# Kernel optimization log

Measured on AMD Instinct MI355X. Metric: run time of the kernel, lower is better.

Reference implementation:

```python
import jax, jax.numpy as jnp
import numpy as np
from jax import lax

NSAMPLE = 16
NEG_SLOPE = 0.1


def leaky(x):
    return jnp.where(x >= 0, x, NEG_SLOPE * x)


def setup_inputs() -> dict:
    key = jax.random.key(0)
    ks = jax.random.split(key, 8)
    B, N1, N2, D = 4, 4096, 4096, 64
    C_in, C_mid, C_out = D + D + 3, 128, 128  # 131 -> 128 -> 128
    xyz1 = jax.random.normal(ks[0], (B, 3, N1), jnp.float32)
    xyz2 = jax.random.normal(ks[1], (B, 3, N2), jnp.float32)
    points1 = jax.random.normal(ks[2], (B, D, N1), jnp.float32)
    points2 = jax.random.normal(ks[3], (B, D, N2), jnp.float32)
    W1 = jax.random.normal(ks[4], (C_mid, C_in), jnp.float32) * 0.05
    b1 = jnp.zeros((C_mid,), jnp.float32)
    W2 = jax.random.normal(ks[5], (C_out, C_mid), jnp.float32) * 0.05
    b2 = jnp.zeros((C_out,), jnp.float32)
    return {"xyz1": xyz1, "xyz2": xyz2, "points1": points1, "points2": points2,
            "W1": W1, "b1": b1, "W2": W2, "b2": b2}


def reference(xyz1, xyz2, points1, points2, W1, b1, W2, b2):
    B, _, N1 = xyz1.shape
    x1 = jnp.transpose(xyz1, (0, 2, 1))      # [B,N1,3]
    x2 = jnp.transpose(xyz2, (0, 2, 1))      # [B,N2,3]
    p1 = jnp.transpose(points1, (0, 2, 1))   # [B,N1,D1]
    p2 = jnp.transpose(points2, (0, 2, 1))   # [B,N2,D2]

    # knn_point: k smallest squared distances from each x1 point into x2
    d2 = (jnp.sum(x1 * x1, -1)[:, :, None]
          + jnp.sum(x2 * x2, -1)[:, None, :]
          - 2.0 * jnp.einsum('bnc,bmc->bnm', x1, x2))  # [B,N1,N2]
    _, knn_idx = lax.top_k(-d2, NSAMPLE)     # [B,N1,K]

    bidx = jnp.arange(B)[:, None, None]
    neighbor_xyz = x2[bidx, knn_idx]         # [B,N1,K,3]
    direction_xyz = neighbor_xyz - x1[:, :, None, :]
    gp2 = p2[bidx, knn_idx]                  # [B,N1,K,D2]
    gp1 = jnp.broadcast_to(p1[:, :, None, :], (B, N1, NSAMPLE, p1.shape[-1]))
    feat = jnp.concatenate([gp1, gp2, direction_xyz], axis=-1)  # [B,N1,K,131]

    h = leaky(jnp.einsum('oc,bnkc->bnko', W1, feat) + b1)
    h = leaky(jnp.einsum('oc,bnkc->bnko', W2, h) + b2)           # [B,N1,K,C_out]

    dist = jnp.maximum(jnp.linalg.norm(direction_xyz, axis=3), 1e-10)  # [B,N1,K]
    inv = 1.0 / dist
    weights = inv / jnp.sum(inv, axis=2, keepdims=True)          # [B,N1,K]

    cost = jnp.einsum('bnk,bnko->bon', weights, h)               # [B,C_out,N1]
    return cost
```

## Files before the change

kernel.cpp:

```cpp
#include <hip/hip_runtime.h>

typedef unsigned short u16;
typedef unsigned int u32;
typedef unsigned long long u64;
typedef __bf16 bf16x8 __attribute__((ext_vector_type(8)));
typedef float f32x4 __attribute__((ext_vector_type(4)));

#define MFMA16(a, b, c) __builtin_amdgcn_mfma_f32_16x16x32_bf16(a, b, c, 0, 0, 0)

static __device__ __forceinline__ u16 f2bf(float f) {
  union { float f; u32 u; } v; v.f = f;
  u32 u = v.u;
  u32 r = (u + 0x7FFFu + ((u >> 16) & 1u)) >> 16;
  return (u16)r;
}

static __device__ __forceinline__ bf16x8 ld16(const u16* p) {
  return __builtin_bit_cast(bf16x8, *(const uint4*)p);
}

static __device__ __forceinline__ u64 u64min(u64 a, u64 b) { return a < b ? a : b; }

static __device__ __forceinline__ u64 bitonic64(u64 v, int lane) {
#pragma unroll
  for (int k = 2; k <= 64; k <<= 1) {
#pragma unroll
    for (int j = k >> 1; j > 0; j >>= 1) {
      u64 o = __shfl_xor(v, j, 64);
      bool up = ((lane & k) == 0);
      bool lower = ((lane & j) == 0);
      u64 mn = v < o ? v : o;
      u64 mx = v < o ? o : v;
      v = (lower == up) ? mn : mx;
    }
  }
  return v;
}

__global__ __launch_bounds__(256) void transpose_cast(const float* __restrict__ src,
                                                      u16* __restrict__ dst) {
  __shared__ __align__(4) u16 tile[64 * 66];
  const int t = threadIdx.x;
  const int b = blockIdx.x >> 6;
  const int n0 = (blockIdx.x & 63) << 6;
  const float* sp = src + ((size_t)b << 18);
#pragma unroll
  for (int i = 0; i < 16; i++) {
    int d = (i << 2) + (t >> 6);
    int n = t & 63;
    tile[n * 66 + d] = f2bf(sp[((size_t)d << 12) + n0 + n]);
  }
  __syncthreads();
  u16* dp = dst + ((size_t)(b * 4096 + n0) << 6);
#pragma unroll
  for (int i = 0; i < 8; i++) {
    int n = (i << 3) + (t >> 5);
    int dp2 = t & 31;
    *(u32*)(dp + n * 64 + (dp2 << 1)) = *(const u32*)(tile + n * 66 + (dp2 << 1));
  }
}

__global__ __launch_bounds__(256) void prep_w(const float* __restrict__ W1,
                                              const float* __restrict__ W2,
                                              u16* __restrict__ W1b,
                                              u16* __restrict__ W2b) {
  int t = blockIdx.x * 256 + threadIdx.x;
  if (t < 128 * 160) {
    int r = t / 160, c = t - r * 160;
    W1b[t] = (c < 131) ? f2bf(W1[r * 131 + c]) : (u16)0;
  } else {
    int u = t - 128 * 160;
    W2b[u] = f2bf(W2[u]);
  }
}

__global__ __launch_bounds__(256) void s2_prep(const float* __restrict__ xyz2,
                                               float* __restrict__ s2) {
  int i = blockIdx.x * 256 + threadIdx.x;
  int b = i >> 12, m = i & 4095;
  const float* X2 = xyz2 + b * 12288;
  float bx = X2[m], by = X2[4096 + m], bz = X2[8192 + m];
  s2[i] = __fadd_rn(__fadd_rn(__fmul_rn(bx, bx), __fmul_rn(by, by)),
                    __fmul_rn(bz, bz));
}

__global__ __launch_bounds__(256, 2) void knn_kernel(const float* __restrict__ xyz1,
                                                     const float* __restrict__ xyz2,
                                                     const float* __restrict__ s2p,
                                                     int* __restrict__ knn) {
  __shared__ float bxL[4096], byL[4096], bzL[4096];
  __shared__ u64 surv[4][64];
  __shared__ u32 cnt[4];
  const int t = threadIdx.x;
  const int lane = t & 63;
  const int w = t >> 6;
  const int b = blockIdx.x >> 7;
  const int rbase = (blockIdx.x & 127) << 5;
  const float* X1 = xyz1 + b * 12288;
  const float* X2 = xyz2 + b * 12288;
  const float* S2 = s2p + b * 4096;

#pragma unroll
  for (int i = 0; i < 4; i++) {
    int e = (i * 256 + t) * 4;
    *(f32x4*)&bxL[e] = *(const f32x4*)&X2[e];
    *(f32x4*)&byL[e] = *(const f32x4*)&X2[4096 + e];
    *(f32x4*)&bzL[e] = *(const f32x4*)&X2[8192 + e];
  }
  __syncthreads();

#pragma unroll 1
  for (int r = 0; r < 8; r++) {
    const int n = rbase + (w << 3) + r;
    const int row = b * 4096 + n;
    const float x = X1[n];
    const float y = X1[4096 + n];
    const float z = X1[8192 + n];
    const float s1 = __fadd_rn(__fadd_rn(__fmul_rn(x, x), __fmul_rn(y, y)),
                               __fmul_rn(z, z));

    u32 keys[64];
    u64 head = ~0ull;
#pragma unroll
    for (int j = 0; j < 64; j++) {
      const int m = (j << 6) + lane;
      float bxv = bxL[m], byv = byL[m], bzv = bzL[m];
      float s2v = S2[m];
      float dt = __builtin_fmaf(z, bzv, __builtin_fmaf(y, byv, __fmul_rn(x, bxv)));
      float d2 = __fsub_rn(__fadd_rn(s1, s2v), __fmul_rn(2.0f, dt));
      u32 bb = __float_as_uint(d2);
      u32 sgn = (u32)((int)bb >> 31);
      u32 key = bb ^ (sgn | 0x80000000u);
      keys[j] = key;
      u64 k64 = ((u64)key << 32) | (u32)m;
      head = head < k64 ? head : k64;
    }

    u64 hs = bitonic64(head, lane);
    u64 tau = __shfl(hs, 15, 64);

    if (lane == 0) cnt[w] = 0;
#pragma unroll
    for (int j = 0; j < 64; j++) {
      u64 k64 = ((u64)keys[j] << 32) | (u32)((j << 6) + lane);
      if (k64 <= tau) {
        u32 slot = atomicAdd(&cnt[w], 1u);
        if (slot < 64) surv[w][slot] = k64;
      }
    }
    u32 S = cnt[w];

    if (S <= 64) {
      u64 v = (lane < (int)S) ? surv[w][lane] : ~0ull;
      v = bitonic64(v, lane);
      if (lane < 16) knn[row * 16 + lane] = (int)(v & 0xFFFFFFFFull);
    } else {
      u64 prev = 0;
      for (int rr = 0; rr < 16; rr++) {
        u64 lm = ~0ull;
#pragma unroll
        for (int j = 0; j < 64; j++) {
          u64 k64 = ((u64)keys[j] << 32) | (u32)((j << 6) + lane);
          if (k64 > prev && k64 < lm) lm = k64;
        }
        u64 gm = lm;
#pragma unroll
        for (int off = 32; off; off >>= 1) gm = u64min(gm, __shfl_xor(gm, off, 64));
        if (lane == 0) knn[row * 16 + rr] = (int)(gm & 0xFFFFFFFFull);
        prev = gm;
      }
    }
  }
}

__global__ __launch_bounds__(256, 3) void mlp_kernel(
    const float* __restrict__ xyz1, const float* __restrict__ xyz2,
    const u16* __restrict__ p1t, const u16* __restrict__ p2t,
    const int* __restrict__ knn,
    const u16* __restrict__ W1b, const float* __restrict__ b1,
    const u16* __restrict__ W2b, const float* __restrict__ b2,
    float* __restrict__ out) {
  __shared__ __align__(16) u16 F[128 * 168];
  __shared__ __align__(16) float winv[128];
  __shared__ __align__(16) float wnorm[128];
  __shared__ __align__(16) float outbuf[128 * 12];
  const int t = threadIdx.x;
  const int g = blockIdx.x;
  const int b = g >> 9;
  const int rbase = (g & 511) << 3;

  {
    const int m = t >> 1, half = t & 1;
    const int n1 = rbase + (m >> 4);
    const uint4* s1p = (const uint4*)(p1t + ((size_t)(b * 4096 + n1) << 6)) + half * 4;
    uint4* d1p = (uint4*)(F + m * 168) + half * 4;
    d1p[0] = s1p[0]; d1p[1] = s1p[1]; d1p[2] = s1p[2]; d1p[3] = s1p[3];
    const int idx = knn[(((size_t)(b * 4096 + n1)) << 4) + (m & 15)];
    const uint4* s2p = (const uint4*)(p2t + ((size_t)(b * 4096 + idx) << 6)) + half * 4;
    uint4* d2p = (uint4*)(F + m * 168 + 64) + half * 4;
    d2p[0] = s2p[0]; d2p[1] = s2p[1]; d2p[2] = s2p[2]; d2p[3] = s2p[3];
  }
  if (t < 128) {
    const int m = t;
    const int n1 = rbase + (m >> 4);
    const int idx = knn[(((size_t)(b * 4096 + n1)) << 4) + (m & 15)];
    const float* X1 = xyz1 + b * 12288;
    const float* X2 = xyz2 + b * 12288;
    float dx = X2[idx] - X1[n1];
    float dy = X2[4096 + idx] - X1[4096 + n1];
    float dz = X2[8192 + idx] - X1[8192 + n1];
    u32 u0 = (u32)f2bf(dx) | ((u32)f2bf(dy) << 16);
    u32 u1 = (u32)f2bf(dz);
    uint4 pk = make_uint4(u0, u1, 0u, 0u);
    *(uint4*)(F + m * 168 + 128) = pk;
    float d = sqrtf(dx * dx + dy * dy + dz * dz);
    winv[m] = 1.0f / fmaxf(d, 1e-10f);
  } else {
    const int m = t - 128;
    uint4 zz = make_uint4(0u, 0u, 0u, 0u);
    uint4* zp = (uint4*)(F + m * 168 + 136);
    zp[0] = zz; zp[1] = zz; zp[2] = zz; zp[3] = zz;
  }
  __syncthreads();

  if (t < 128) {
    const int r = t >> 4;
    float s = 0.f;
#pragma unroll
    for (int k = 0; k < 16; k++) s += winv[(r << 4) + k];
    wnorm[t] = winv[t] / s;
  }

  const int lane = t & 63;
  const int wid = t >> 6;
  const int l15 = lane & 15;
  const int quad = lane >> 4;
  const int koff = quad << 3;
  const int nbase = wid << 5;

  f32x4 acc[8][2];
  const f32x4 z4 = {0.f, 0.f, 0.f, 0.f};
#pragma unroll
  for (int i = 0; i < 8; i++)
#pragma unroll
    for (int j = 0; j < 2; j++) acc[i][j] = z4;

#pragma unroll
  for (int s = 0; s < 5; s++) {
    bf16x8 bf0 = ld16(W1b + (nbase + l15) * 160 + s * 32 + koff);
    bf16x8 bf1 = ld16(W1b + (nbase + 16 + l15) * 160 + s * 32 + koff);
#pragma unroll
    for (int mt = 0; mt < 8; mt++) {
      bf16x8 a = ld16(F + (mt * 16 + l15) * 168 + s * 32 + koff);
      acc[mt][0] = MFMA16(a, bf0, acc[mt][0]);
      acc[mt][1] = MFMA16(a, bf1, acc[mt][1]);
    }
  }
  __syncthreads();

  {
    const float bv0 = b1[nbase + l15];
    const float bv1 = b1[nbase + 16 + l15];
#pragma unroll
    for (int mt = 0; mt < 8; mt++) {
      u16* hrow = F + (mt * 16 + quad * 4) * 168;
#pragma unroll
      for (int r = 0; r < 4; r++) {
        float zv0 = acc[mt][0][r] + bv0;
        zv0 = (zv0 >= 0.f) ? zv0 : 0.1f * zv0;
        hrow[r * 168 + nbase + l15] = f2bf(zv0);
        float zv1 = acc[mt][1][r] + bv1;
        zv1 = (zv1 >= 0.f) ? zv1 : 0.1f * zv1;
        hrow[r * 168 + nbase + 16 + l15] = f2bf(zv1);
      }
    }
  }
  __syncthreads();

  f32x4 acc2[8][2];
#pragma unroll
  for (int i = 0; i < 8; i++)
#pragma unroll
    for (int j = 0; j < 2; j++) acc2[i][j] = z4;

#pragma unroll
  for (int s = 0; s < 4; s++) {
    bf16x8 bf0 = ld16(W2b + (nbase + l15) * 128 + s * 32 + koff);
    bf16x8 bf1 = ld16(W2b + (nbase + 16 + l15) * 128 + s * 32 + koff);
#pragma unroll
    for (int mt = 0; mt < 8; mt++) {
      bf16x8 a = ld16(F + (mt * 16 + l15) * 168 + s * 32 + koff);
      acc2[mt][0] = MFMA16(a, bf0, acc2[mt][0]);
      acc2[mt][1] = MFMA16(a, bf1, acc2[mt][1]);
    }
  }

  {
    const float bv0 = b2[nbase + l15];
    const float bv1 = b2[nbase + 16 + l15];
#pragma unroll
    for (int mt = 0; mt < 8; mt++) {
      const f32x4 w4 = *(const f32x4*)&wnorm[(mt << 4) + (quad << 2)];
      float p0 = 0.f, p1 = 0.f;
#pragma unroll
      for (int r = 0; r < 4; r++) {
        float zv0 = acc2[mt][0][r] + bv0;
        zv0 = (zv0 >= 0.f) ? zv0 : 0.1f * zv0;
        p0 += zv0 * w4[r];
        float zv1 = acc2[mt][1][r] + bv1;
        zv1 = (zv1 >= 0.f) ? zv1 : 0.1f * zv1;
        p1 += zv1 * w4[r];
      }
      p0 += __shfl_xor(p0, 16); p0 += __shfl_xor(p0, 32);
      p1 += __shfl_xor(p1, 16); p1 += __shfl_xor(p1, 32);
      if (quad == 0) {
        outbuf[(nbase + l15) * 12 + mt] = p0;
        outbuf[(nbase + 16 + l15) * 12 + mt] = p1;
      }
    }
  }
  __syncthreads();
  {
    const int ch = t >> 1, half = t & 1;
    f32x4 v = *(const f32x4*)&outbuf[ch * 12 + (half << 2)];
    float* op = out + (((size_t)(b * 128 + ch)) << 12) + rbase + (half << 2);
    *(f32x4*)op = v;
  }
}

extern "C" void kernel_launch(void* const* d_in, const int* in_sizes, int n_in,
                              void* d_out, int out_size, void* d_ws, size_t ws_size,
                              hipStream_t stream) {
  const float* xyz1 = (const float*)d_in[0];
  const float* xyz2 = (const float*)d_in[1];
  const float* points1 = (const float*)d_in[2];
  const float* points2 = (const float*)d_in[3];
  const float* W1 = (const float*)d_in[4];
  const float* b1 = (const float*)d_in[5];
  const float* W2 = (const float*)d_in[6];
  const float* b2 = (const float*)d_in[7];
  float* out = (float*)d_out;

  char* ws = (char*)d_ws;
  int* knn = (int*)ws;
  u16* p1t = (u16*)(ws + 1048576);
  u16* p2t = (u16*)(ws + 3145728);
  u16* W1b = (u16*)(ws + 5242880);
  u16* W2b = (u16*)(ws + 5283840);
  float* s2 = (float*)(ws + 5316608);

  hipLaunchKernelGGL(transpose_cast, dim3(256), dim3(256), 0, stream, points1, p1t);
  hipLaunchKernelGGL(transpose_cast, dim3(256), dim3(256), 0, stream, points2, p2t);
  hipLaunchKernelGGL(prep_w, dim3(144), dim3(256), 0, stream, W1, W2, W1b, W2b);
  hipLaunchKernelGGL(s2_prep, dim3(64), dim3(256), 0, stream, xyz2, s2);
  hipLaunchKernelGGL(knn_kernel, dim3(512), dim3(256), 0, stream, xyz1, xyz2, s2, knn);
  hipLaunchKernelGGL(mlp_kernel, dim3(2048), dim3(256), 0, stream,
                     xyz1, xyz2, p1t, p2t, knn, W1b, b1, W2b, b2, out);
}
```

Baseline: 174.1 us.

## Process two query rows per pass in knn with packed float4 candidates

Fuses the squared-norm precompute into the knn kernel and stores candidates in shared memory as packed (x,y,z,s2) float4. Each wave now computes distances for two query points per pass, so every shared-memory load serves two rows. Threshold selection uses a float bitonic sort instead of a 64-bit one. This doubles the per-thread key arrays, which raises register pressure and may reduce occupancy.

```diff
diff --git a/kernel.cpp b/kernel.cpp
--- a/kernel.cpp
+++ b/kernel.cpp
@@ -35,6 +35,34 @@
     }
   }
   return v;
+}
+
+static __device__ __forceinline__ float bitonic64f(float v, int lane) {
+#pragma unroll
+  for (int k = 2; k <= 64; k <<= 1) {
+#pragma unroll
+    for (int j = k >> 1; j > 0; j >>= 1) {
+      float o = __shfl_xor(v, j, 64);
+      bool up = ((lane & k) == 0);
+      bool lower = ((lane & j) == 0);
+      float mn = fminf(v, o);
+      float mx = fmaxf(v, o);
+      v = (lower == up) ? mn : mx;
+    }
+  }
+  return v;
+}
+
+static __device__ __forceinline__ u32 fkey(float f) {
+  u32 bb = __float_as_uint(f);
+  u32 sgn = (u32)((int)bb >> 31);
+  return bb ^ (sgn | 0x80000000u);
+}
+
+static __device__ __forceinline__ float d2of(float x, float y, float z, float s1,
+                                             f32x4 c) {
+  float dt = __builtin_fmaf(z, c[2], __builtin_fmaf(y, c[1], __fmul_rn(x, c[0])));
+  return __fsub_rn(__fadd_rn(s1, c[3]), __fmul_rn(2.0f, dt));
 }
 
 __global__ __launch_bounds__(256) void transpose_cast(const float* __restrict__ src,
@@ -74,21 +102,10 @@
   }
 }
 
-__global__ __launch_bounds__(256) void s2_prep(const float* __restrict__ xyz2,
-                                               float* __restrict__ s2) {
-  int i = blockIdx.x * 256 + threadIdx.x;
-  int b = i >> 12, m = i & 4095;
-  const float* X2 = xyz2 + b * 12288;
-  float bx = X2[m], by = X2[4096 + m], bz = X2[8192 + m];
-  s2[i] = __fadd_rn(__fadd_rn(__fmul_rn(bx, bx), __fmul_rn(by, by)),
-                    __fmul_rn(bz, bz));
-}
-
 __global__ __launch_bounds__(256, 2) void knn_kernel(const float* __restrict__ xyz1,
                                                      const float* __restrict__ xyz2,
-                                                     const float* __restrict__ s2p,
                                                      int* __restrict__ knn) {
-  __shared__ float bxL[4096], byL[4096], bzL[4096];
+  __shared__ __align__(16) float candL[4096 * 4];
   __shared__ u64 surv[4][64];
   __shared__ u32 cnt[4];
   const int t = threadIdx.x;
@@ -98,76 +115,107 @@
   const int rbase = (blockIdx.x & 127) << 5;
   const float* X1 = xyz1 + b * 12288;
   const float* X2 = xyz2 + b * 12288;
-  const float* S2 = s2p + b * 4096;
-
-#pragma unroll
-  for (int i = 0; i < 4; i++) {
-    int e = (i * 256 + t) * 4;
-    *(f32x4*)&bxL[e] = *(const f32x4*)&X2[e];
-    *(f32x4*)&byL[e] = *(const f32x4*)&X2[4096 + e];
-    *(f32x4*)&bzL[e] = *(const f32x4*)&X2[8192 + e];
+
+#pragma unroll
+  for (int j2 = 0; j2 < 16; j2++) {
+    int m = j2 * 256 + t;
+    float x = X2[m], y = X2[4096 + m], z = X2[8192 + m];
+    float s2 = __fadd_rn(__fadd_rn(__fmul_rn(x, x), __fmul_rn(y, y)),
+                         __fmul_rn(z, z));
+    f32x4 pk = {x, y, z, s2};
+    *(f32x4*)&candL[m * 4] = pk;
   }
   __syncthreads();
 
 #pragma unroll 1
-  for (int r = 0; r < 8; r++) {
-    const int n = rbase + (w << 3) + r;
-    const int row = b * 4096 + n;
-    const float x = X1[n];
-    const float y = X1[4096 + n];
-    const float z = X1[8192 + n];
-    const float s1 = __fadd_rn(__fadd_rn(__fmul_rn(x, x), __fmul_rn(y, y)),
-                               __fmul_rn(z, z));
-
-    u32 keys[64];
-    u64 head = ~0ull;
+  for (int p = 0; p < 4; p++) {
+    const int nA = rbase + (w << 3) + p * 2;
+    const int nB = nA + 1;
+    const float xA = X1[nA], yA = X1[4096 + nA], zA = X1[8192 + nA];
+    const float xB = X1[nB], yB = X1[4096 + nB], zB = X1[8192 + nB];
+    const float s1A = __fadd_rn(__fadd_rn(__fmul_rn(xA, xA), __fmul_rn(yA, yA)),
+                                __fmul_rn(zA, zA));
+    const float s1B = __fadd_rn(__fadd_rn(__fmul_rn(xB, xB), __fmul_rn(yB, yB)),
+                                __fmul_rn(zB, zB));
+
+    float kA[64], kB[64];
+    float fmA = 3e38f, fmB = 3e38f;
 #pragma unroll
     for (int j = 0; j < 64; j++) {
       const int m = (j << 6) + lane;
-      float bxv = bxL[m], byv = byL[m], bzv = bzL[m];
-      float s2v = S2[m];
-      float dt = __builtin_fmaf(z, bzv, __builtin_fmaf(y, byv, __fmul_rn(x, bxv)));
-      float d2 = __fsub_rn(__fadd_rn(s1, s2v), __fmul_rn(2.0f, dt));
-      u32 bb = __float_as_uint(d2);
-      u32 sgn = (u32)((int)bb >> 31);
-      u32 key = bb ^ (sgn | 0x80000000u);
-      keys[j] = key;
-      u64 k64 = ((u64)key << 32) | (u32)m;
-      head = head < k64 ? head : k64;
-    }
-
-    u64 hs = bitonic64(head, lane);
-    u64 tau = __shfl(hs, 15, 64);
-
-    if (lane == 0) cnt[w] = 0;
-#pragma unroll
-    for (int j = 0; j < 64; j++) {
-      u64 k64 = ((u64)keys[j] << 32) | (u32)((j << 6) + lane);
-      if (k64 <= tau) {
-        u32 slot = atomicAdd(&cnt[w], 1u);
-        if (slot < 64) surv[w][slot] = k64;
-      }
-    }
-    u32 S = cnt[w];
-
-    if (S <= 64) {
-      u64 v = (lane < (int)S) ? surv[w][lane] : ~0ull;
-      v = bitonic64(v, lane);
-      if (lane < 16) knn[row * 16 + lane] = (int)(v & 0xFFFFFFFFull);
-    } else {
-      u64 prev = 0;
-      for (int rr = 0; rr < 16; rr++) {
-        u64 lm = ~0ull;
-#pragma unroll
-        for (int j = 0; j < 64; j++) {
-          u64 k64 = ((u64)keys[j] << 32) | (u32)((j << 6) + lane);
-          if (k64 > prev && k64 < lm) lm = k64;
+      f32x4 c = *(const f32x4*)&candL[m * 4];
+      float dA = d2of(xA, yA, zA, s1A, c);
+      float dB = d2of(xB, yB, zB, s1B, c);
+      kA[j] = dA; fmA = fminf(fmA, dA);
+      kB[j] = dB; fmB = fminf(fmB, dB);
+    }
+
+    {
+      float tauf = __shfl(bitonic64f(fmA, lane), 15, 64);
+      if (lane == 0) cnt[w] = 0;
+#pragma unroll
+      for (int j = 0; j < 64; j++) {
+        if (kA[j] <= tauf) {
+          u64 k64 = ((u64)fkey(kA[j]) << 32) | (u32)((j << 6) + lane);
+          u32 slot = atomicAdd(&cnt[w], 1u);
+          if (slot < 64) surv[w][slot] = k64;
         }
-        u64 gm = lm;
-#pragma unroll
-        for (int off = 32; off; off >>= 1) gm = u64min(gm, __shfl_xor(gm, off, 64));
-        if (lane == 0) knn[row * 16 + rr] = (int)(gm & 0xFFFFFFFFull);
-        prev = gm;
+      }
+      u32 S = cnt[w];
+      const int row = b * 4096 + nA;
+      if (S <= 64) {
+        u64 v = (lane < (int)S) ? surv[w][lane] : ~0ull;
+        v = bitonic64(v, lane);
+        if (lane < 16) knn[row * 16 + lane] = (int)(v & 0xFFFFFFFFull);
+      } else {
+        u64 prev = 0;
+        for (int rr = 0; rr < 16; rr++) {
+          u64 lm = ~0ull;
+#pragma unroll
+          for (int j = 0; j < 64; j++) {
+            u64 k64 = ((u64)fkey(kA[j]) << 32) | (u32)((j << 6) + lane);
+            if (k64 > prev && k64 < lm) lm = k64;
+          }
+          u64 gm = lm;
+#pragma unroll
+          for (int off = 32; off; off >>= 1) gm = u64min(gm, __shfl_xor(gm, off, 64));
+          if (lane == 0) knn[row * 16 + rr] = (int)(gm & 0xFFFFFFFFull);
+          prev = gm;
+        }
+      }
+    }
+    {
+      float tauf = __shfl(bitonic64f(fmB, lane), 15, 64);
+      if (lane == 0) cnt[w] = 0;
+#pragma unroll
+      for (int j = 0; j < 64; j++) {
+        if (kB[j] <= tauf) {
+          u64 k64 = ((u64)fkey(kB[j]) << 32) | (u32)((j << 6) + lane);
+          u32 slot = atomicAdd(&cnt[w], 1u);
+          if (slot < 64) surv[w][slot] = k64;
+        }
+      }
+      u32 S = cnt[w];
+      const int row = b * 4096 + nB;
+      if (S <= 64) {
+        u64 v = (lane < (int)S) ? surv[w][lane] : ~0ull;
+        v = bitonic64(v, lane);
+        if (lane < 16) knn[row * 16 + lane] = (int)(v & 0xFFFFFFFFull);
+      } else {
+        u64 prev = 0;
+        for (int rr = 0; rr < 16; rr++) {
+          u64 lm = ~0ull;
+#pragma unroll
+          for (int j = 0; j < 64; j++) {
+            u64 k64 = ((u64)fkey(kB[j]) << 32) | (u32)((j << 6) + lane);
+            if (k64 > prev && k64 < lm) lm = k64;
+          }
+          u64 gm = lm;
+#pragma unroll
+          for (int off = 32; off; off >>= 1) gm = u64min(gm, __shfl_xor(gm, off, 64));
+          if (lane == 0) knn[row * 16 + rr] = (int)(gm & 0xFFFFFFFFull);
+          prev = gm;
+        }
       }
     }
   }
@@ -347,13 +395,11 @@
   u16* p2t = (u16*)(ws + 3145728);
   u16* W1b = (u16*)(ws + 5242880);
   u16* W2b = (u16*)(ws + 5283840);
-  float* s2 = (float*)(ws + 5316608);
 
   hipLaunchKernelGGL(transpose_cast, dim3(256), dim3(256), 0, stream, points1, p1t);
   hipLaunchKernelGGL(transpose_cast, dim3(256), dim3(256), 0, stream, points2, p2t);
   hipLaunchKernelGGL(prep_w, dim3(144), dim3(256), 0, stream, W1, W2, W1b, W2b);
-  hipLaunchKernelGGL(s2_prep, dim3(64), dim3(256), 0, stream, xyz2, s2);
-  hipLaunchKernelGGL(knn_kernel, dim3(512), dim3(256), 0, stream, xyz1, xyz2, s2, knn);
+  hipLaunchKernelGGL(knn_kernel, dim3(512), dim3(256), 0, stream, xyz1, xyz2, knn);
   hipLaunchKernelGGL(mlp_kernel, dim3(2048), dim3(256), 0, stream,
                      xyz1, xyz2, p1t, p2t, knn, W1b, b1, W2b, b2, out);
 }
```

After: 274.1 us. 1.57x slower.
